# Kernel optimization log

Measured on AMD Instinct MI355X. Metric: run time of the kernel, lower is better.

The kernel has to match this reference:

```python
import jax, jax.numpy as jnp
import numpy as np

B, C, H, W = 4, 256, 224, 224
WH = WW = 8
SH = SW = 4
HEADS = 8
HD = C // HEADS
N = WH * WW
EPS = 1e-5


def _rel_index():
    coords = np.stack(np.meshgrid(np.arange(WH), np.arange(WW), indexing='ij')).reshape(2, -1)
    rel = (coords[:, :, None] - coords[:, None, :]).transpose(1, 2, 0).copy()
    rel[:, :, 0] += WH - 1
    rel[:, :, 1] += WW - 1
    rel[:, :, 0] *= 2 * WW - 1
    return rel.sum(-1)  # (N, N) int

REL_INDEX = _rel_index()


def _shift_mask(Hp, Wp):
    # Swin shift mask for one image: (nW, N, N) float, 0 or -100
    img = np.zeros((Hp, Wp))
    cnt = 0
    for a, b in [(0, Hp - WH), (Hp - WH, Hp - SH), (Hp - SH, Hp)]:
        for c, d in [(0, Wp - WW), (Wp - WW, Wp - SW), (Wp - SW, Wp)]:
            img[a:b, c:d] = cnt
            cnt += 1
    mw = img.reshape(Hp // WH, WH, Wp // WW, WW).transpose(0, 2, 1, 3).reshape(-1, N)
    diff = mw[:, None, :] - mw[:, :, None]  # [w, i, j] = mw[w,j] - mw[w,i]
    return np.where(diff != 0, np.float32(-100.0), np.float32(0.0)).astype(np.float32)


def _ln(x, w, b):
    m = jnp.mean(x, axis=-1, keepdims=True)
    v = jnp.mean(jnp.square(x - m), axis=-1, keepdims=True)
    return (x - m) * jax.lax.rsqrt(v + EPS) * w + b


def setup_inputs() -> dict:
    key = jax.random.key(0)
    ks = jax.random.split(key, 8)
    num_rel = (2 * WH - 1) * (2 * WW - 1)
    return {
        'x': jax.random.normal(ks[0], (B, C, H, W), dtype=jnp.float32),
        'qkv_w': jax.random.normal(ks[1], (3 * C, C), dtype=jnp.float32) * 0.02,
        'proj_w': jax.random.normal(ks[2], (C, C), dtype=jnp.float32) * 0.02,
        'proj_b': jnp.zeros((C,), dtype=jnp.float32),
        'rpb_table': jax.random.normal(ks[3], (num_rel, HEADS), dtype=jnp.float32) * 0.02,
        'norm1_w': jnp.ones((C,), dtype=jnp.float32),
        'norm1_b': jnp.zeros((C,), dtype=jnp.float32),
        'norm2_w': jnp.ones((C,), dtype=jnp.float32),
        'norm2_b': jnp.zeros((C,), dtype=jnp.float32),
        'mlp_w1': jax.random.normal(ks[4], (4 * C, C), dtype=jnp.float32) * 0.02,
        'mlp_b1': jnp.zeros((4 * C,), dtype=jnp.float32),
        'mlp_w2': jax.random.normal(ks[5], (C, 4 * C), dtype=jnp.float32) * 0.02,
        'mlp_b2': jnp.zeros((C,), dtype=jnp.float32),
    }


def reference(x, qkv_w, proj_w, proj_b, rpb_table, norm1_w, norm1_b,
              norm2_w, norm2_b, mlp_w1, mlp_b1, mlp_w2, mlp_b2):
    Bx, Cx, Hx, Wx = x.shape
    pad_h = (WH - Hx % WH) % WH
    pad_w = (WW - Wx % WW) % WW
    if pad_h or pad_w:
        x = jnp.pad(x, ((0, 0), (0, 0), (0, pad_h), (0, pad_w)))
    Hp, Wp = Hx + pad_h, Wx + pad_w
    x = jnp.transpose(x, (0, 2, 3, 1))                    # BHWC
    x = jnp.roll(x, (-SH, -SW), axis=(1, 2))
    nW = (Hp // WH) * (Wp // WW)
    # window partition -> (B*nW, N, C), batch-major
    xw = x.reshape(Bx, Hp // WH, WH, Wp // WW, WW, Cx)
    xw = jnp.transpose(xw, (0, 1, 3, 2, 4, 5)).reshape(-1, N, Cx)

    # ----- windowed attention -----
    h = _ln(xw, norm1_w, norm1_b)
    qkv = (h @ qkv_w.T).reshape(-1, N, 3, HEADS, HD)
    qkv = jnp.transpose(qkv, (2, 0, 3, 1, 4))             # (3, Bw, heads, N, hd)
    q, k, v = qkv[0], qkv[1], qkv[2]
    attn = jnp.einsum('bhnd,bhmd->bhnm', q, k) * (1.0 / HD ** 0.5)
    bias = jnp.transpose(rpb_table[REL_INDEX.reshape(-1)].reshape(N, N, HEADS), (2, 0, 1))
    attn = attn + bias[None]
    # faithful to torch: repeat_interleave(B, dim=0) -> window-major mask ordering
    mask = jnp.asarray(_shift_mask(Hp, Wp))               # (nW, N, N)
    attn = attn + jnp.repeat(mask, Bx, axis=0)[:, None]
    attn = jax.nn.softmax(attn, axis=-1)
    out = jnp.einsum('bhnm,bhmd->bhnd', attn, v)
    out = jnp.transpose(out, (0, 2, 1, 3)).reshape(-1, N, Cx)
    out = out @ proj_w.T + proj_b
    xw = xw + out

    # ----- MLP -----
    h = _ln(xw, norm2_w, norm2_b)
    h = jax.nn.gelu(h @ mlp_w1.T + mlp_b1, approximate=False) @ mlp_w2.T + mlp_b2
    xw = xw + h

    # window reverse, un-shift, un-pad
    x = xw.reshape(Bx, Hp // WH, Wp // WW, WH, WW, Cx)
    x = jnp.transpose(x, (0, 1, 3, 2, 4, 5)).reshape(Bx, Hp, Wp, Cx)
    x = jnp.roll(x, (SH, SW), axis=(1, 2))
    x = x[:, :Hx, :Wx, :]
    return jnp.transpose(x, (0, 3, 1, 2))
```

## Files before the change

### kernel.cpp

```cpp
#include <hip/hip_runtime.h>

typedef unsigned short u16;
typedef unsigned int   u32;
typedef __attribute__((ext_vector_type(8))) __bf16 bf16x8;
typedef __attribute__((ext_vector_type(4))) float  f32x4;
typedef __attribute__((ext_vector_type(4))) u16    u16x4;

#define DEV __device__ __forceinline__

DEV u16 f2b(float f) {
  union { float f; u32 u; } a; a.f = f;
  const u32 u = a.u;
  return (u16)((u + 0x7fffu + ((u >> 16) & 1u)) >> 16);
}

DEV float gelu_fast(float x) {
  const float x2 = x * x;
  const float t  = __builtin_fmaf(0.1029430f, x2, 2.3022150f);
  const float e  = __builtin_exp2f(x * t);
  const float r  = __builtin_amdgcn_rcpf(1.0f + e);
  return __builtin_fmaf(-x, r, x);
}

DEV void gload16(const void* g, void* l) {
  __builtin_amdgcn_global_load_lds(
      (const __attribute__((address_space(1))) void*)g,
      (__attribute__((address_space(3))) void*)l, 16, 0, 0);
}

__global__ __launch_bounds__(256)
void conv_weights(const float* __restrict__ qkvw, const float* __restrict__ projw,
                  const float* __restrict__ w1,   const float* __restrict__ w2,
                  u16* __restrict__ dq, u16* __restrict__ dp,
                  u16* __restrict__ d1, u16* __restrict__ d2) {
  const int t = blockIdx.x * 256 + threadIdx.x;
  if (t < 196608)      dq[t]          = f2b(qkvw[t]);
  else if (t < 262144) dp[t - 196608] = f2b(projw[t - 196608]);
  else if (t < 524288) d1[t - 262144] = f2b(w1[t - 262144]);
  else                 d2[t - 524288] = f2b(w2[t - 524288]);
}

__global__ __launch_bounds__(256)
void ln1_win(const float* __restrict__ x, const float* __restrict__ w1,
             const float* __restrict__ b1, u16* __restrict__ hout,
             float* __restrict__ xwout) {
  __shared__ float xt[64 * 257];
  __shared__ float smean[256], srstd[256];
  const int tid = threadIdx.x, lane = tid & 63, wv = tid >> 6;
  const int g = blockIdx.x;
  const int b = g / 196, rem = g % 196;
  const int wh = rem / 7, wg = rem % 7;
  const int base_r = b * 784 + wh * 28 + wg * 4;
  const int pr = tid >> 5, pc = tid & 31;
  int hp = wh * 8 + 4 + pr; if (hp >= 224) hp -= 224;
  int wp = wg * 32 + 4 + pc; if (wp >= 224) wp -= 224;
  const long roff = (long)b * 256 * 50176 + hp * 224 + wp;

  float s = 0.f, q = 0.f;
  for (int cc = 0; cc < 4; ++cc) {
#pragma unroll 8
    for (int i = 0; i < 64; ++i) {
      const int c = cc * 64 + i;
      const float v = x[(long)c * 50176 + roff];
      xt[i * 257 + tid] = v;
      s += v; q += v * v;
    }
    __syncthreads();
#pragma unroll 8
    for (int jj = 0; jj < 64; ++jj) {
      const int p = jj * 4 + wv;
      const int m = (base_r + ((p & 31) >> 3)) * 64 + (p >> 5) * 8 + (p & 7);
      xwout[(long)m * 256 + cc * 64 + lane] = xt[lane * 257 + p];
    }
    __syncthreads();
  }
  const float mean = s * (1.f / 256.f);
  smean[tid] = mean;
  srstd[tid] = rsqrtf(q * (1.f / 256.f) - mean * mean + 1e-5f);
  __syncthreads();

  float wr_[4], br_[4];
#pragma unroll
  for (int cc = 0; cc < 4; ++cc) { wr_[cc] = w1[cc * 64 + lane]; br_[cc] = b1[cc * 64 + lane]; }
#pragma unroll 2
  for (int jj = 0; jj < 64; ++jj) {
    const int p = jj * 4 + wv;
    const int m = (base_r + ((p & 31) >> 3)) * 64 + (p >> 5) * 8 + (p & 7);
    const float mu = smean[p], rs = srstd[p];
#pragma unroll
    for (int cc = 0; cc < 4; ++cc) {
      const float v = xwout[(long)m * 256 + cc * 64 + lane];
      hout[(long)m * 256 + cc * 64 + lane] = f2b((v - mu) * rs * wr_[cc] + br_[cc]);
    }
  }
}

template<int EPI, int NCOL>
__global__ __launch_bounds__(512, 4)
void gemm_bt(const u16* __restrict__ A, const u16* __restrict__ Bw, const int K,
             float* __restrict__ fout, const float* __restrict__ bias,
             u16* __restrict__ bout,
             const float* __restrict__ lnw, const float* __restrict__ lnb) {
  __shared__ __align__(16) u16 smem[24576];
  u16* sA0 = smem;
  u16* sB0 = smem + 4096;
  u16* sA1 = smem + 12288;
  u16* sB1 = smem + 16384;

  const int tid  = threadIdx.x;
  const int lane = tid & 63;
  const int wid  = tid >> 6;
  const int wrr  = wid >> 2;
  const int wcc  = wid & 3;

  const int nwg = gridDim.x;
  const int bid = blockIdx.x;
  const int wg  = (bid & 7) * (nwg >> 3) + (bid >> 3);
  const int row0 = wg * 128;

  const f32x4 vzero = {0.f, 0.f, 0.f, 0.f};

  const int l15  = lane & 15;
  const int l4   = lane >> 4;
  const int ksw2 = (l15 >> 1) & 3;
  const int lcol = (((tid & 3) ^ ((tid >> 3) & 3)) << 3);

  const u16* pA = A + (long)(row0 + (tid >> 2)) * K + lcol;
  const int wbase = wid * 512;

#define STAGE_TILE(KT, DA, DB)                  \
  {                                             \
    gload16(pA  + (KT), (DA) + wbase);          \
    gload16(pB  + (KT), (DB) + wbase);          \
    gload16(pB2 + (KT), (DB) + 4096 + wbase);   \
  }

#define COMPUTE_TILE(SA, SB, SWAP)                                                      \
  {                                                                                     \
    bf16x8 af[4], bfv[4];                                                               \
    _Pragma("unroll")                                                                   \
    for (int mi = 0; mi < 4; ++mi)                                                      \
      af[mi] = *(const bf16x8*)((SA) + (wrr * 64 + mi * 16 + l15) * 32 +                \
                                ((l4 ^ ksw2) << 3));                                    \
    _Pragma("unroll")                                                                   \
    for (int nj = 0; nj < 4; ++nj)                                                      \
      bfv[nj] = *(const bf16x8*)((SB) + (wcc * 64 + nj * 16 + l15) * 32 +               \
                                 ((l4 ^ ksw2) << 3));                                   \
    _Pragma("unroll")                                                                   \
    for (int mi = 0; mi < 4; ++mi)                                                      \
      _Pragma("unroll")                                                                 \
      for (int nj = 0; nj < 4; ++nj) {                                                  \
        if (SWAP)                                                                       \
          acc[mi][nj] = __builtin_amdgcn_mfma_f32_16x16x32_bf16(bfv[nj], af[mi],        \
                                                                acc[mi][nj], 0, 0, 0);  \
        else                                                                            \
          acc[mi][nj] = __builtin_amdgcn_mfma_f32_16x16x32_bf16(af[mi], bfv[nj],        \
                                                                acc[mi][nj], 0, 0, 0);  \
      }                                                                                 \
  }

#define KLOOP(SWAP)                                                  \
  {                                                                  \
    const int nt = K >> 5;                                           \
    STAGE_TILE(0, sA0, sB0);                                         \
    int cur = 0;                                                     \
    for (int t = 0; t < nt; ++t) {                                   \
      u16* cA = cur ? sA1 : sA0;                                     \
      u16* cB = cur ? sB1 : sB0;                                     \
      u16* nA = cur ? sA0 : sA1;                                     \
      u16* nB = cur ? sB0 : sB1;                                     \
      if (t + 1 < nt) {                                              \
        STAGE_TILE((t + 1) << 5, nA, nB);                            \
        asm volatile("s_waitcnt vmcnt(3)" ::: "memory");             \
      } else {                                                       \
        asm volatile("s_waitcnt vmcnt(0)" ::: "memory");             \
      }                                                              \
      __builtin_amdgcn_s_barrier();                                  \
      asm volatile("" ::: "memory");                                 \
      COMPUTE_TILE(cA, cB, SWAP);                                    \
      asm volatile("" ::: "memory");                                 \
      __builtin_amdgcn_s_barrier();                                  \
      cur ^= 1;                                                      \
    }                                                                \
  }

#pragma unroll
  for (int cb = 0; cb < NCOL; ++cb) {
    const int col0 = cb * 256;
    const u16* pB  = Bw + (long)(col0 + (tid >> 2)) * K + lcol;
    const u16* pB2 = pB + (long)128 * K;

    f32x4 acc[4][4];
#pragma unroll
    for (int i = 0; i < 4; ++i)
#pragma unroll
      for (int j = 0; j < 4; ++j) acc[i][j] = vzero;

    if (EPI == 0 && cb == 2) {
      KLOOP(0);
#pragma unroll
      for (int mi = 0; mi < 4; ++mi) {
        const int mb = row0 + wrr * 64 + mi * 16 + (l4 << 2);
        const int rrg = mb >> 6, ii = mb & 63;
#pragma unroll
        for (int nj = 0; nj < 4; ++nj) {
          const int n = 512 + wcc * 64 + nj * 16 + l15;
          const int hh = (n >> 5) & 7, d = n & 31;
          u16x4 p;
#pragma unroll
          for (int reg = 0; reg < 4; ++reg) p[reg] = f2b(acc[mi][nj][reg]);
          *(u16x4*)(bout + 102760448L + (long)((rrg * 8 + hh) * 32 + d) * 64 + ii) = p;
        }
      }
      continue;
    }

    KLOOP(1);

    if (EPI == 0) {
#pragma unroll
      for (int mi = 0; mi < 4; ++mi) {
        const int m = row0 + wrr * 64 + mi * 16 + l15;
        const int rr = m >> 6, ii = m & 63;
#pragma unroll
        for (int nj = 0; nj < 4; ++nj) {
          const int n = col0 + wcc * 64 + nj * 16 + (l4 << 2);
          const int s = n >> 8, hh = (n >> 5) & 7, d = n & 31;
          u16x4 p;
#pragma unroll
          for (int reg = 0; reg < 4; ++reg) p[reg] = f2b(acc[mi][nj][reg]);
          *(u16x4*)(bout + (long)s * 51380224L +
                    (long)((rr * 8 + hh) * 64 + ii) * 32 + d) = p;
        }
      }
    } else if (EPI == 1) {
      f32x4 b4[4];
#pragma unroll
      for (int nj = 0; nj < 4; ++nj)
        b4[nj] = *(const f32x4*)(bias + wcc * 64 + nj * 16 + (l4 << 2));
      float sS[4], sQ[4];
#pragma unroll
      for (int mi = 0; mi < 4; ++mi) {
        const int m = row0 + wrr * 64 + mi * 16 + l15;
        float* yrow = fout + (long)m * 256;
        float s = 0.f, q = 0.f;
#pragma unroll
        for (int nj = 0; nj < 4; ++nj) {
          const int n = wcc * 64 + nj * 16 + (l4 << 2);
          f32x4 o = *(f32x4*)(yrow + n);
#pragma unroll
          for (int reg = 0; reg < 4; ++reg) {
            o[reg] += acc[mi][nj][reg] + b4[nj][reg];
            s += o[reg]; q += o[reg] * o[reg];
          }
          *(f32x4*)(yrow + n) = o;
          acc[mi][nj] = o;
        }
        s += __shfl_xor(s, 16); s += __shfl_xor(s, 32);
        q += __shfl_xor(q, 16); q += __shfl_xor(q, 32);
        sS[mi] = s; sQ[mi] = q;
      }
      float* ps = (float*)smem;
      float* pq = ps + 512;
      __syncthreads();
      if (lane < 16) {
#pragma unroll
        for (int mi = 0; mi < 4; ++mi) {
          const int idx = (wrr * 64 + mi * 16 + l15) * 4 + wcc;
          ps[idx] = sS[mi]; pq[idx] = sQ[mi];
        }
      }
      __syncthreads();
#pragma unroll
      for (int mi = 0; mi < 4; ++mi) {
        const int m = row0 + wrr * 64 + mi * 16 + l15;
        const int base = (wrr * 64 + mi * 16 + l15) * 4;
        const float S = ps[base] + ps[base + 1] + ps[base + 2] + ps[base + 3];
        const float Q = pq[base] + pq[base + 1] + pq[base + 2] + pq[base + 3];
        const float mean = S * (1.f / 256.f);
        const float rstd = rsqrtf(Q * (1.f / 256.f) - mean * mean + 1e-5f);
#pragma unroll
        for (int nj = 0; nj < 4; ++nj) {
          const int n = wcc * 64 + nj * 16 + (l4 << 2);
          const f32x4 w4 = *(const f32x4*)(lnw + n);
          const f32x4 c4 = *(const f32x4*)(lnb + n);
          u16x4 p;
#pragma unroll
          for (int reg = 0; reg < 4; ++reg)
            p[reg] = f2b((acc[mi][nj][reg] - mean) * rstd * w4[reg] + c4[reg]);
          *(u16x4*)(bout + (long)m * 256 + n) = p;
        }
      }
    }
  }
#undef STAGE_TILE
#undef COMPUTE_TILE
#undef KLOOP
}

__global__ __launch_bounds__(512, 2)
void mlp_fused(const u16* __restrict__ A, const u16* __restrict__ w1b,
               const u16* __restrict__ w2b, const float* __restrict__ y,
               const float* __restrict__ b1, const float* __restrict__ b2,
               float* __restrict__ oout) {
  __shared__ __align__(16) u16 smem[57344];
  u16* sA0 = smem;
  u16* sB0 = smem + 4096;
  u16* sA1 = smem + 12288;
  u16* sB1 = smem + 16384;
  u16* H   = smem + 24576;

  const int tid  = threadIdx.x;
  const int lane = tid & 63;
  const int wid  = tid >> 6;
  const int wrr  = wid >> 2;
  const int wcc  = wid & 3;

  const int nwg = gridDim.x;
  const int bid = blockIdx.x;
  const int wg  = (bid & 7) * (nwg >> 3) + (bid >> 3);
  const int row0 = wg * 128;

  const f32x4 vzero = {0.f, 0.f, 0.f, 0.f};
  const int l15  = lane & 15;
  const int l4   = lane >> 4;
  const int ksw2 = (l15 >> 1) & 3;
  const int lcol = (((tid & 3) ^ ((tid >> 3) & 3)) << 3);

  const u16* pA = A + (long)(row0 + (tid >> 2)) * 256 + lcol;
  const int wbase = wid * 512;

  f32x4 acc2[4][4];
#pragma unroll
  for (int i = 0; i < 4; ++i)
#pragma unroll
    for (int j = 0; j < 4; ++j) acc2[i][j] = vzero;

#define RD_FRAG(BUF, R0, OFF) \
  (*(const bf16x8*)((BUF) + ((R0) + l15) * 32 + ((l4 ^ ksw2) << 3) + (OFF)))

  for (int cb = 0; cb < 4; ++cb) {
    const u16* pB  = w1b + (long)(cb * 256 + (tid >> 2)) * 256 + lcol;
    const u16* pB2 = pB + 128 * 256;

    f32x4 acc[4][4];
#pragma unroll
    for (int i = 0; i < 4; ++i)
#pragma unroll
      for (int j = 0; j < 4; ++j) acc[i][j] = vzero;

    {
      gload16(pA, sA0 + wbase);
      gload16(pB, sB0 + wbase);
      gload16(pB2, sB0 + 4096 + wbase);
      int cur = 0;
      for (int t = 0; t < 8; ++t) {
        u16* cA = cur ? sA1 : sA0;
        u16* cB = cur ? sB1 : sB0;
        u16* nA = cur ? sA0 : sA1;
        u16* nB = cur ? sB0 : sB1;
        if (t + 1 < 8) {
          const int kt = (t + 1) << 5;
          gload16(pA + kt, nA + wbase);
          gload16(pB + kt, nB + wbase);
          gload16(pB2 + kt, nB + 4096 + wbase);
          asm volatile("s_waitcnt vmcnt(3)" ::: "memory");
        } else {
          asm volatile("s_waitcnt vmcnt(0)" ::: "memory");
        }
        __builtin_amdgcn_s_barrier();
        asm volatile("" ::: "memory");
        {
          bf16x8 af[4], bfv[4];
#pragma unroll
          for (int mi = 0; mi < 4; ++mi) af[mi] = RD_FRAG(cA, wrr * 64 + mi * 16, 0);
#pragma unroll
          for (int nj = 0; nj < 4; ++nj) bfv[nj] = RD_FRAG(cB, wcc * 64 + nj * 16, 0);
#pragma unroll
          for (int mi = 0; mi < 4; ++mi)
#pragma unroll
            for (int nj = 0; nj < 4; ++nj)
              acc[mi][nj] = __builtin_amdgcn_mfma_f32_16x16x32_bf16(
                  bfv[nj], af[mi], acc[mi][nj], 0, 0, 0);
        }
        asm volatile("" ::: "memory");
        __builtin_amdgcn_s_barrier();
        cur ^= 1;
      }
    }

    const u16* qB  = w2b + (long)(tid >> 2) * 1024 + cb * 256 + lcol;
    const u16* qB2 = qB + 128 * 1024;
    gload16(qB, sB0 + wbase);
    gload16(qB2, sB0 + 4096 + wbase);

    {
      f32x4 b4[4];
#pragma unroll
      for (int nj = 0; nj < 4; ++nj)
        b4[nj] = *(const f32x4*)(b1 + cb * 256 + wcc * 64 + nj * 16 + (l4 << 2));
#pragma unroll
      for (int mi = 0; mi < 4; ++mi) {
        const int m = wrr * 64 + mi * 16 + l15;
#pragma unroll
        for (int nj = 0; nj < 4; ++nj) {
          u16x4 p;
#pragma unroll
          for (int reg = 0; reg < 4; ++reg)
            p[reg] = f2b(gelu_fast(acc[mi][nj][reg] + b4[nj][reg]));
          const int kt   = wcc * 2 + (nj >> 1);
          const int slot = ((nj & 1) << 1) + (l4 >> 1);
          *(u16x4*)(H + kt * 4096 + m * 32 +
                    ((slot ^ ((m >> 1) & 3)) << 3) + ((l4 & 1) << 2)) = p;
        }
      }
    }
    __syncthreads();

    {
      int cur = 0;
      for (int kt = 0; kt < 8; ++kt) {
        u16* cB = cur ? sB1 : sB0;
        u16* nB = cur ? sB0 : sB1;
        if (kt + 1 < 8) {
          const int ko = (kt + 1) << 5;
          gload16(qB + ko, nB + wbase);
          gload16(qB2 + ko, nB + 4096 + wbase);
          asm volatile("s_waitcnt vmcnt(2)" ::: "memory");
        } else {
          asm volatile("s_waitcnt vmcnt(0)" ::: "memory");
        }
        __builtin_amdgcn_s_barrier();
        asm volatile("" ::: "memory");
        {
          const u16* Hk = H + kt * 4096;
          bf16x8 af[4], bfv[4];
#pragma unroll
          for (int mi = 0; mi < 4; ++mi) af[mi] = RD_FRAG(Hk, wrr * 64 + mi * 16, 0);
#pragma unroll
          for (int nj = 0; nj < 4; ++nj) bfv[nj] = RD_FRAG(cB, wcc * 64 + nj * 16, 0);
#pragma unroll
          for (int mi = 0; mi < 4; ++mi)
#pragma unroll
            for (int nj = 0; nj < 4; ++nj)
              acc2[mi][nj] = __builtin_amdgcn_mfma_f32_16x16x32_bf16(
                  bfv[nj], af[mi], acc2[mi][nj], 0, 0, 0);
        }
        asm volatile("" ::: "memory");
        __builtin_amdgcn_s_barrier();
        cur ^= 1;
      }
    }
    __syncthreads();
  }
#undef RD_FRAG

  {
    f32x4 b4[4];
#pragma unroll
    for (int nj = 0; nj < 4; ++nj)
      b4[nj] = *(const f32x4*)(b2 + wcc * 64 + nj * 16 + (l4 << 2));
#pragma unroll
    for (int mi = 0; mi < 4; ++mi) {
      const int m = row0 + wrr * 64 + mi * 16 + l15;
      const float* yrow = y + (long)m * 256;
#pragma unroll
      for (int nj = 0; nj < 4; ++nj) {
        const int n = wcc * 64 + nj * 16 + (l4 << 2);
        const f32x4 yv = *(const f32x4*)(yrow + n);
#pragma unroll
        for (int reg = 0; reg < 4; ++reg)
          acc2[mi][nj][reg] += yv[reg] + b4[nj][reg];
      }
    }
    const int wr0 = row0 >> 6;
    const int b = wr0 / 784, rem = wr0 % 784;
    const int wh = rem / 28, wwb = rem % 28;
    float* tp = (float*)smem;
    const int pidx = tid & 127, cgrp = tid >> 7;
    const int pr = pidx >> 4, pc = pidx & 15;
    int hp = wh * 8 + 4 + pr;  if (hp >= 224) hp -= 224;
    int wp = wwb * 8 + 4 + pc; if (wp >= 224) wp -= 224;
    float* ob = oout + (long)b * 256 * 50176 + hp * 224 + wp;
#pragma unroll
    for (int cc = 0; cc < 4; ++cc) {
      __syncthreads();
      if (wcc == cc) {
#pragma unroll
        for (int mi = 0; mi < 4; ++mi) {
          const int ml = wrr * 64 + mi * 16 + l15;
          const int px = ((ml & 63) >> 3) * 16 + (ml >> 6) * 8 + (ml & 7);
#pragma unroll
          for (int nj = 0; nj < 4; ++nj)
#pragma unroll
            for (int reg = 0; reg < 4; ++reg)
              tp[(nj * 16 + (l4 << 2) + reg) * 128 + (px ^ (l4 << 2))] =
                  acc2[mi][nj][reg];
        }
      }
      __syncthreads();
#pragma unroll 4
      for (int j = 0; j < 16; ++j) {
        const int cl = cgrp * 16 + j;
        ob[(long)(cc * 64 + cl) * 50176] =
            tp[cl * 128 + (pidx ^ (((cl >> 2) & 3) << 2))];
      }
    }
  }
}

__global__ __launch_bounds__(256)
void attn_win(const u16* __restrict__ qkv, const float* __restrict__ rpb,
              u16* __restrict__ aout) {
  __shared__ u16 Pl[4][4096];
  __shared__ float srpb[1800];
  const int tid = threadIdx.x, lane = tid & 63, wv = tid >> 6;
  const int bid = blockIdx.x;
  const int r = bid >> 1;
  const int h = (bid & 1) * 4 + wv;
  for (int i = tid; i < 1800; i += 256) srpb[i] = rpb[i];
  __syncthreads();

  const int midx = r >> 2;
  const int wh = midx / 28, ww = midx % 28;
  const int l15 = lane & 15, l4 = lane >> 4;

  u16* Pw = &Pl[wv][0];
  const long hb = (long)(r * 8 + h) * 2048;
  const u16* qh = qkv + hb;
  const u16* kh = qkv + 51380224 + hb;
  const u16* vh = qkv + 102760448 + hb;

  int rj[4], cj[4], labj[4];
#pragma unroll
  for (int nj = 0; nj < 4; ++nj) {
    const int j = nj * 16 + l15;
    rj[nj] = j >> 3; cj[nj] = j & 7;
    const int hp = wh * 8 + rj[nj], wp = ww * 8 + cj[nj];
    const int lh = (hp < 216) ? 0 : ((hp < 220) ? 1 : 2);
    const int lw = (wp < 216) ? 0 : ((wp < 220) ? 1 : 2);
    labj[nj] = lh * 3 + lw;
  }

  const f32x4 vzero = {0.f, 0.f, 0.f, 0.f};

  bf16x8 qf[4], kf[4];
#pragma unroll
  for (int mi = 0; mi < 4; ++mi)
    qf[mi] = *(const bf16x8*)(qh + (mi * 16 + l15) * 32 + l4 * 8);
#pragma unroll
  for (int nj = 0; nj < 4; ++nj)
    kf[nj] = *(const bf16x8*)(kh + (nj * 16 + l15) * 32 + l4 * 8);

  f32x4 S[4][4];
#pragma unroll
  for (int mi = 0; mi < 4; ++mi)
#pragma unroll
    for (int nj = 0; nj < 4; ++nj)
      S[mi][nj] = __builtin_amdgcn_mfma_f32_16x16x32_bf16(qf[mi], kf[nj], vzero, 0, 0, 0);

#pragma unroll
  for (int mi = 0; mi < 4; ++mi)
#pragma unroll
    for (int reg = 0; reg < 4; ++reg) {
      const int i = mi * 16 + (l4 << 2) + reg;
      const int ri = i >> 3, ci = i & 7;
      const int hp = wh * 8 + ri, wp = ww * 8 + ci;
      const int lh = (hp < 216) ? 0 : ((hp < 220) ? 1 : 2);
      const int lw = (wp < 216) ? 0 : ((wp < 220) ? 1 : 2);
      const int li = lh * 3 + lw;
      float v[4];
#pragma unroll
      for (int nj = 0; nj < 4; ++nj) {
        const int idx = (ri - rj[nj] + 7) * 15 + (ci - cj[nj] + 7);
        v[nj] = S[mi][nj][reg] * 0.17677669529663687f + srpb[idx * 8 + h]
              + ((li != labj[nj]) ? -100.0f : 0.0f);
      }
      float mx = fmaxf(fmaxf(v[0], v[1]), fmaxf(v[2], v[3]));
      mx = fmaxf(mx, __shfl_xor(mx, 1));
      mx = fmaxf(mx, __shfl_xor(mx, 2));
      mx = fmaxf(mx, __shfl_xor(mx, 4));
      mx = fmaxf(mx, __shfl_xor(mx, 8));
      float sum = 0.f;
#pragma unroll
      for (int nj = 0; nj < 4; ++nj) { v[nj] = __expf(v[nj] - mx); sum += v[nj]; }
      sum += __shfl_xor(sum, 1);
      sum += __shfl_xor(sum, 2);
      sum += __shfl_xor(sum, 4);
      sum += __shfl_xor(sum, 8);
      const float rinv = __builtin_amdgcn_rcpf(sum);
      const int sw = (i & 7) << 3;
#pragma unroll
      for (int nj = 0; nj < 4; ++nj)
        Pw[i * 64 + ((nj * 16 + l15) ^ sw)] = f2b(v[nj] * rinv);
    }

  f32x4 OT[2][4];
#pragma unroll
  for (int td = 0; td < 2; ++td)
#pragma unroll
    for (int ti = 0; ti < 4; ++ti) OT[td][ti] = vzero;

  const int rsw = (l15 & 7) << 3;
#pragma unroll
  for (int kk = 0; kk < 2; ++kk) {
    bf16x8 pf[4], vf[2];
#pragma unroll
    for (int ti = 0; ti < 4; ++ti)
      pf[ti] = *(const bf16x8*)(Pw + (ti * 16 + l15) * 64 + ((kk * 32 + l4 * 8) ^ rsw));
#pragma unroll
    for (int td = 0; td < 2; ++td)
      vf[td] = *(const bf16x8*)(vh + (td * 16 + l15) * 64 + kk * 32 + l4 * 8);
#pragma unroll
    for (int td = 0; td < 2; ++td)
#pragma unroll
      for (int ti = 0; ti < 4; ++ti)
        OT[td][ti] = __builtin_amdgcn_mfma_f32_16x16x32_bf16(vf[td], pf[ti], OT[td][ti], 0, 0, 0);
  }

#pragma unroll
  for (int td = 0; td < 2; ++td)
#pragma unroll
    for (int ti = 0; ti < 4; ++ti) {
      const int i = ti * 16 + l15;
      const int d0 = td * 16 + (l4 << 2);
      u16x4 p;
#pragma unroll
      for (int reg = 0; reg < 4; ++reg) p[reg] = f2b(OT[td][ti][reg]);
      *(u16x4*)(aout + (long)(r * 64 + i) * 256 + h * 32 + d0) = p;
    }
}

extern "C" void kernel_launch(void* const* d_in, const int* in_sizes, int n_in,
                              void* d_out, int out_size, void* d_ws, size_t ws_size,
                              hipStream_t stream) {
  (void)in_sizes; (void)n_in; (void)out_size; (void)ws_size;
  const float* x     = (const float*)d_in[0];
  const float* qkvw  = (const float*)d_in[1];
  const float* projw = (const float*)d_in[2];
  const float* projb = (const float*)d_in[3];
  const float* rpb   = (const float*)d_in[4];
  const float* n1w   = (const float*)d_in[5];
  const float* n1b   = (const float*)d_in[6];
  const float* n2w   = (const float*)d_in[7];
  const float* n2b   = (const float*)d_in[8];
  const float* w1    = (const float*)d_in[9];
  const float* b1    = (const float*)d_in[10];
  const float* w2    = (const float*)d_in[11];
  const float* b2    = (const float*)d_in[12];

  char* ws = (char*)d_ws;
  u16*   hbuf   = (u16*)(ws);
  u16*   qkvb   = (u16*)(ws + 102760448);
  u16*   abuf   = (u16*)(ws + 411041792);
  float* ybuf   = (float*)(ws + 513802240);
  u16*   qkvwb  = (u16*)(ws + 719323136);
  u16*   projwb = (u16*)(ws + 719716352);
  u16*   w1b    = (u16*)(ws + 719847424);
  u16*   w2b    = (u16*)(ws + 720371712);

  conv_weights<<<3072, 256, 0, stream>>>(qkvw, projw, w1, w2, qkvwb, projwb, w1b, w2b);
  ln1_win<<<784, 256, 0, stream>>>(x, n1w, n1b, hbuf, ybuf);
  gemm_bt<0, 3><<<1568, 512, 0, stream>>>(hbuf, qkvwb, 256, nullptr, nullptr, qkvb, nullptr, nullptr);
  attn_win<<<6272, 256, 0, stream>>>(qkvb, rpb, abuf);
  gemm_bt<1, 1><<<1568, 512, 0, stream>>>(abuf, projwb, 256, ybuf, projb, hbuf, n2w, n2b);
  mlp_fused<<<1568, 512, 0, stream>>>(hbuf, w1b, w2b, ybuf, b1, b2, (float*)d_out);
}
```

Measured before the change: 1.052 ms.

## Load MLP GEMM operands directly from global memory instead of staging through LDS

Removes the double-buffered LDS staging of the A tile and the W1/W2 weight tiles in the fused MLP kernel. Each wave now loads its MFMA fragments straight from global memory, and only the hidden activation H stays in shared memory. With the smaller LDS footprint the launch bound rises to allow 4 blocks per CU, and the per-step barriers go away. The cost is that fragments are no longer shared across waves, so global and L2 traffic rises and load latency is no longer hidden by explicit prefetch. Register pressure under the higher occupancy target could also force spills.

Result: slower. 1.762 ms (+67.5%).

```diff
diff --git a/kernel.cpp b/kernel.cpp
--- a/kernel.cpp
+++ b/kernel.cpp
@@ -298,17 +298,13 @@
 #undef KLOOP
 }
 
-__global__ __launch_bounds__(512, 2)
+__global__ __launch_bounds__(512, 4)
 void mlp_fused(const u16* __restrict__ A, const u16* __restrict__ w1b,
                const u16* __restrict__ w2b, const float* __restrict__ y,
                const float* __restrict__ b1, const float* __restrict__ b2,
                float* __restrict__ oout) {
-  __shared__ __align__(16) u16 smem[57344];
-  u16* sA0 = smem;
-  u16* sB0 = smem + 4096;
-  u16* sA1 = smem + 12288;
-  u16* sB1 = smem + 16384;
-  u16* H   = smem + 24576;
+  __shared__ __align__(16) u16 smem[32768];
+  u16* H = smem;
 
   const int tid  = threadIdx.x;
   const int lane = tid & 63;
@@ -325,10 +321,10 @@
   const int l15  = lane & 15;
   const int l4   = lane >> 4;
   const int ksw2 = (l15 >> 1) & 3;
-  const int lcol = (((tid & 3) ^ ((tid >> 3) & 3)) << 3);
-
-  const u16* pA = A + (long)(row0 + (tid >> 2)) * 256 + lcol;
-  const int wbase = wid * 512;
+
+  const u16* pA = A + (long)(row0 + wrr * 64 + l15) * 256 + l4 * 8;
+  const u16* pW1 = w1b + (long)(wcc * 64 + l15) * 256 + l4 * 8;
+  const u16* pW2 = w2b + (long)(wcc * 64 + l15) * 1024 + l4 * 8;
 
   f32x4 acc2[4][4];
 #pragma unroll
@@ -336,12 +332,8 @@
 #pragma unroll
     for (int j = 0; j < 4; ++j) acc2[i][j] = vzero;
 
-#define RD_FRAG(BUF, R0, OFF) \
-  (*(const bf16x8*)((BUF) + ((R0) + l15) * 32 + ((l4 ^ ksw2) << 3) + (OFF)))
-
   for (int cb = 0; cb < 4; ++cb) {
-    const u16* pB  = w1b + (long)(cb * 256 + (tid >> 2)) * 256 + lcol;
-    const u16* pB2 = pB + 128 * 256;
+    const u16* pB1 = pW1 + (long)cb * 256 * 256;
 
     f32x4 acc[4][4];
 #pragma unroll
@@ -349,50 +341,22 @@
 #pragma unroll
       for (int j = 0; j < 4; ++j) acc[i][j] = vzero;
 
-    {
-      gload16(pA, sA0 + wbase);
-      gload16(pB, sB0 + wbase);
-      gload16(pB2, sB0 + 4096 + wbase);
-      int cur = 0;
-      for (int t = 0; t < 8; ++t) {
-        u16* cA = cur ? sA1 : sA0;
-        u16* cB = cur ? sB1 : sB0;
-        u16* nA = cur ? sA0 : sA1;
-        u16* nB = cur ? sB0 : sB1;
-        if (t + 1 < 8) {
-          const int kt = (t + 1) << 5;
-          gload16(pA + kt, nA + wbase);
-          gload16(pB + kt, nB + wbase);
-          gload16(pB2 + kt, nB + 4096 + wbase);
-          asm volatile("s_waitcnt vmcnt(3)" ::: "memory");
-        } else {
-          asm volatile("s_waitcnt vmcnt(0)" ::: "memory");
-        }
-        __builtin_amdgcn_s_barrier();
-        asm volatile("" ::: "memory");
-        {
-          bf16x8 af[4], bfv[4];
-#pragma unroll
-          for (int mi = 0; mi < 4; ++mi) af[mi] = RD_FRAG(cA, wrr * 64 + mi * 16, 0);
-#pragma unroll
-          for (int nj = 0; nj < 4; ++nj) bfv[nj] = RD_FRAG(cB, wcc * 64 + nj * 16, 0);
-#pragma unroll
-          for (int mi = 0; mi < 4; ++mi)
-#pragma unroll
-            for (int nj = 0; nj < 4; ++nj)
-              acc[mi][nj] = __builtin_amdgcn_mfma_f32_16x16x32_bf16(
-                  bfv[nj], af[mi], acc[mi][nj], 0, 0, 0);
-        }
-        asm volatile("" ::: "memory");
-        __builtin_amdgcn_s_barrier();
-        cur ^= 1;
-      }
-    }
-
-    const u16* qB  = w2b + (long)(tid >> 2) * 1024 + cb * 256 + lcol;
-    const u16* qB2 = qB + 128 * 1024;
-    gload16(qB, sB0 + wbase);
-    gload16(qB2, sB0 + 4096 + wbase);
+#pragma unroll
+    for (int kt = 0; kt < 8; ++kt) {
+      bf16x8 af[4], bfv[4];
+#pragma unroll
+      for (int mi = 0; mi < 4; ++mi)
+        af[mi] = *(const bf16x8*)(pA + (long)(mi * 16) * 256 + kt * 32);
+#pragma unroll
+      for (int nj = 0; nj < 4; ++nj)
+        bfv[nj] = *(const bf16x8*)(pB1 + (long)(nj * 16) * 256 + kt * 32);
+#pragma unroll
+      for (int mi = 0; mi < 4; ++mi)
+#pragma unroll
+        for (int nj = 0; nj < 4; ++nj)
+          acc[mi][nj] = __builtin_amdgcn_mfma_f32_16x16x32_bf16(
+              bfv[nj], af[mi], acc[mi][nj], 0, 0, 0);
+    }
 
     {
       f32x4 b4[4];
@@ -418,42 +382,28 @@
     __syncthreads();
 
     {
-      int cur = 0;
+      const u16* pB2 = pW2 + cb * 256;
+#pragma unroll
       for (int kt = 0; kt < 8; ++kt) {
-        u16* cB = cur ? sB1 : sB0;
-        u16* nB = cur ? sB0 : sB1;
-        if (kt + 1 < 8) {
-          const int ko = (kt + 1) << 5;
-          gload16(qB + ko, nB + wbase);
-          gload16(qB2 + ko, nB + 4096 + wbase);
-          asm volatile("s_waitcnt vmcnt(2)" ::: "memory");
-        } else {
-          asm volatile("s_waitcnt vmcnt(0)" ::: "memory");
-        }
-        __builtin_amdgcn_s_barrier();
-        asm volatile("" ::: "memory");
-        {
-          const u16* Hk = H + kt * 4096;
-          bf16x8 af[4], bfv[4];
-#pragma unroll
-          for (int mi = 0; mi < 4; ++mi) af[mi] = RD_FRAG(Hk, wrr * 64 + mi * 16, 0);
-#pragma unroll
-          for (int nj = 0; nj < 4; ++nj) bfv[nj] = RD_FRAG(cB, wcc * 64 + nj * 16, 0);
-#pragma unroll
-          for (int mi = 0; mi < 4; ++mi)
-#pragma unroll
-            for (int nj = 0; nj < 4; ++nj)
-              acc2[mi][nj] = __builtin_amdgcn_mfma_f32_16x16x32_bf16(
-                  bfv[nj], af[mi], acc2[mi][nj], 0, 0, 0);
-        }
-        asm volatile("" ::: "memory");
-        __builtin_amdgcn_s_barrier();
-        cur ^= 1;
+        const u16* Hk = H + kt * 4096;
+        bf16x8 af[4], bfv[4];
+#pragma unroll
+        for (int mi = 0; mi < 4; ++mi)
+          af[mi] = *(const bf16x8*)(Hk + (wrr * 64 + mi * 16 + l15) * 32 +
+                                    ((l4 ^ ksw2) << 3));
+#pragma unroll
+        for (int nj = 0; nj < 4; ++nj)
+          bfv[nj] = *(const bf16x8*)(pB2 + (long)(nj * 16) * 1024 + kt * 32);
+#pragma unroll
+        for (int mi = 0; mi < 4; ++mi)
+#pragma unroll
+          for (int nj = 0; nj < 4; ++nj)
+            acc2[mi][nj] = __builtin_amdgcn_mfma_f32_16x16x32_bf16(
+                bfv[nj], af[mi], acc2[mi][nj], 0, 0, 0);
       }
     }
     __syncthreads();
   }
-#undef RD_FRAG
 
   {
     f32x4 b4[4];
```
